# Optimization experiments

Measured on AMD Instinct MI355X. Metric: run time of the kernel, lower is better.

## Reference

```python
import jax, jax.numpy as jnp
import numpy as np

D = 1024
N_HEAD = 16
D_HEAD = D // N_HEAD
EPS = 1e-6


def setup_inputs() -> dict:
    key = jax.random.key(0)
    k1, k2, k3 = jax.random.split(key, 3)
    x = jax.random.normal(k1, (4, 1024, D), dtype=jnp.float32)
    # Linear weights stored as (in, out); y = x @ W
    Wqkv = jax.random.normal(k2, (D, 3 * D), dtype=jnp.float32) * (1.0 / np.sqrt(D))
    Wo = jax.random.normal(k3, (D, D), dtype=jnp.float32) * (1.0 / np.sqrt(D))
    scale_q = jnp.ones((D_HEAD,), dtype=jnp.float32)
    scale_k = jnp.ones((D_HEAD,), dtype=jnp.float32)
    return {"x": x, "Wqkv": Wqkv, "Wo": Wo, "scale_q": scale_q, "scale_k": scale_k}


def _rmsnorm_global(x, scale):
    # NOTE: faithful to source: mean over ALL elements (scalar RMS), not per-vector.
    rms = jnp.sqrt(jnp.mean(x * x))
    return (x / (rms + EPS)) * scale  # scale broadcasts over last dim (d_head)


def reference(x, Wqkv, Wo, scale_q, scale_k):
    b, s, d = x.shape
    qkv = x @ Wqkv  # (b, s, 3d)
    q, k, v = jnp.split(qkv, 3, axis=-1)
    q = q.reshape(b, s, N_HEAD, D_HEAD)
    k = k.reshape(b, s, N_HEAD, D_HEAD)
    v = v.reshape(b, s, N_HEAD, D_HEAD)
    q = _rmsnorm_global(q, scale_q)
    k = _rmsnorm_global(k, scale_k)
    # NOTE: no 1/sqrt(d_head) scaling, no mask (faithful to source)
    attn = jnp.einsum('bqhd,bkhd->bhqk', q, k)
    attn = jax.nn.softmax(attn, axis=-1)
    z = jnp.einsum('bhqk,bkhd->bqhd', attn, v)
    z = z.reshape(b, s, d)
    return z @ Wo
```

## Files before the change

kernel.cpp:

```cpp
#include <hip/hip_runtime.h>

typedef float f32x4 __attribute__((ext_vector_type(4)));
typedef short bf16x8 __attribute__((ext_vector_type(8)));
typedef _Float16 f16x8 __attribute__((ext_vector_type(8)));
typedef unsigned short u16;

__device__ __forceinline__ u16 f2bf(float f) {
  unsigned int u = __float_as_uint(f);
  u = u + 0x7fffu + ((u >> 16) & 1u);
  return (u16)(u >> 16);
}
__device__ __forceinline__ float bf2f(u16 h) {
  return __uint_as_float(((unsigned int)h) << 16);
}
__device__ __forceinline__ u16 f2h(float f) {
  _Float16 h = (_Float16)f;
  union { _Float16 h; u16 u; } cv;
  cv.h = h;
  return cv.u;
}

typedef unsigned int as1_uint __attribute__((address_space(1)));
typedef unsigned int as3_uint __attribute__((address_space(3)));
__device__ __forceinline__ void gl_lds16(const void* g, void* l) {
  __builtin_amdgcn_global_load_lds((as1_uint*)g, (as3_uint*)l, 16, 0, 0);
}


__global__ __launch_bounds__(256) void conv_x_kernel(const float* __restrict__ x,
                                                     u16* __restrict__ Xp) {
  const int g = blockIdx.x * 256 + threadIdx.x;
  const int o = g * 8;
  const int slab = o >> 17;
  const int rem = o & 131071;
  const int kstep = rem >> 12;
  const int rem2 = rem & 4095;
  const int r = rem2 >> 5;
  const int cp = (rem2 & 31) >> 3;
  const int c = cp ^ ((r >> 1) & 3);
  const int s = slab * 128 + r;
  const int k = kstep * 32 + c * 8;
  const float4 v0 = *(const float4*)&x[(size_t)s * 1024 + k];
  const float4 v1 = *(const float4*)&x[(size_t)s * 1024 + k + 4];
  ushort4 a, b;
  a.x = f2h(v0.x); a.y = f2h(v0.y); a.z = f2h(v0.z); a.w = f2h(v0.w);
  b.x = f2h(v1.x); b.y = f2h(v1.y); b.z = f2h(v1.z); b.w = f2h(v1.w);
  *(ushort4*)&Xp[o] = a;
  *(ushort4*)&Xp[o + 4] = b;
}

__global__ __launch_bounds__(256) void conv_w_kernel(
    const float* __restrict__ src, int ncols, u16* __restrict__ dst) {
  __shared__ float tl[64][132];
  const int t = threadIdx.x;
  const int slab = blockIdx.x, kg = blockIdx.y;
  const int n0 = slab * 128, k0 = kg * 64;
#pragma unroll
  for (int i = 0; i < 8; i++) {
    const int fidx = i * 256 + t;
    const int r = fidx >> 5, c4 = (fidx & 31) * 4;
    *(float4*)&tl[r][c4] = *(const float4*)&src[(size_t)(k0 + r) * ncols + n0 + c4];
  }
  __syncthreads();
  const size_t base = (size_t)slab * 131072 + (size_t)(kg * 2) * 4096;
#pragma unroll
  for (int i = 0; i < 4; i++) {
    const int g = i * 256 + t;
    const int img = g >> 9, ci = g & 511;
    const int r = ci >> 2, cp = ci & 3;
    const int c = cp ^ ((r >> 1) & 3);
    const int klc = img * 32 + c * 8;
    ushort4 h0, h1;
    float v[8];
#pragma unroll
    for (int e = 0; e < 8; e++) v[e] = tl[klc + e][r];
    h0.x = f2h(v[0]); h0.y = f2h(v[1]); h0.z = f2h(v[2]); h0.w = f2h(v[3]);
    h1.x = f2h(v[4]); h1.y = f2h(v[5]); h1.z = f2h(v[6]); h1.w = f2h(v[7]);
    *(ushort4*)&dst[base + g * 8] = h0;
    *(ushort4*)&dst[base + g * 8 + 4] = h1;
  }
}

__global__ __launch_bounds__(512, 2) void gemm_qkv_kernel(
    const u16* __restrict__ Xp, const u16* __restrict__ Wp,
    u16* __restrict__ qf, u16* __restrict__ kf, u16* __restrict__ vT,
    const float* __restrict__ scale_q, const float* __restrict__ scale_k,
    float* __restrict__ sums) {
  __shared__ u16 SA[2][4][4096];
  __shared__ u16 SB[2][4][4096];
  const int tid = threadIdx.x, wv = tid >> 6, lane = tid & 63;
  const int lm = lane & 15, quad = lane >> 4;
  const int wvM = wv >> 2, wvN = wv & 3;
  const int L = blockIdx.x;
  const int xcd = L & 7, idx = L >> 3;
  const int bmT = (xcd & 3) * 4 + (idx & 3);
  const int bnT = (xcd >> 2) * 6 + (idx >> 2);
  const bool is_v = (bnT >= 8);
  const int fq = (quad ^ ((lm >> 1) & 3)) * 8;
  const int aOff = lm * 32 + fq;
  const u16* Xg = Xp + (size_t)bmT * 262144;
  const u16* Wg = Wp + (size_t)bnT * 262144;
  int bSub[4];
#pragma unroll
  for (int n = 0; n < 4; n++) {
    const int wn = wvN * 64 + n * 16;
    bSub[n] = ((wn >> 7) * 4096) + (wn & 127) * 32;
  }
  const u16* Ard = is_v ? &SA[0][0][0] : &SB[0][0][0];
  const u16* Brd = is_v ? &SB[0][0][0] : &SA[0][0][0];

  const f32x4 z4 = {0.f, 0.f, 0.f, 0.f};
  f32x4 acc[8][4];
#pragma unroll
  for (int i = 0; i < 8; i++)
#pragma unroll
    for (int j = 0; j < 4; j++) acc[i][j] = z4;

#define VMCNT4() asm volatile("s_waitcnt vmcnt(4)" ::: "memory")
#define VMCNT0() asm volatile("s_waitcnt vmcnt(0)" ::: "memory")
#define LGKM0() asm volatile("s_waitcnt lgkmcnt(0)" ::: "memory")
#define CFENCE() asm volatile("" ::: "memory")
#define SP1() __builtin_amdgcn_s_setprio(1)
#define SP0() __builtin_amdgcn_s_setprio(0)

#define QSTAGE(tt, nb, k2, sl)                                               \
  do {                                                                       \
    const size_t go_ = (size_t)(sl)*131072 + (size_t)(2 * (tt) + (k2)) * 4096\
                       + wv * 512 + lane * 8;                                \
    gl_lds16(Xg + go_, &SA[nb][(k2)*2 + (sl)][wv * 512]);                    \
    gl_lds16(Wg + go_, &SB[nb][(k2)*2 + (sl)][wv * 512]);                    \
  } while (0)

#define READ_A(BUF, k2, mq)                                                  \
  _Pragma("unroll")                                                          \
  for (int i = 0; i < 4; i++)                                                \
    afr[i] = *(const f16x8*)&Ard[(BUF)*16384 + ((k2)*2 + wvM) * 4096 +       \
                                 ((mq)*4 + i) * 512 + aOff];
#define READ_B(BUF, k2)                                                      \
  _Pragma("unroll")                                                          \
  for (int n = 0; n < 4; n++)                                                \
    bfr[n] = *(const f16x8*)&Brd[(BUF)*16384 + (k2)*8192 + bSub[n] + aOff];
#define MFMA16(mq)                                                           \
  _Pragma("unroll")                                                          \
  for (int i = 0; i < 4; i++)                                                \
    _Pragma("unroll")                                                        \
    for (int n = 0; n < 4; n++)                                              \
      acc[(mq)*4 + i][n] = __builtin_amdgcn_mfma_f32_16x16x32_f16(           \
          afr[i], bfr[n], acc[(mq)*4 + i][n], 0, 0, 0);

#define PH_WAIT_MFMA(mq)                                                     \
  CFENCE();                                                                  \
  __builtin_amdgcn_s_barrier();                                              \
  CFENCE();                                                                  \
  LGKM0();                                                                   \
  __builtin_amdgcn_sched_barrier(0);                                         \
  SP1();                                                                     \
  MFMA16(mq);                                                                \
  SP0()

#define KTILE(BUF, NBUF, t, DOSTAGE, GATE1, GATE3)                           \
  do {                                                                       \
    f16x8 bfr[4];                                                            \
    {                                                  \
      f16x8 afr[4];                                                          \
      READ_A(BUF, 0, 0);                                                     \
      READ_B(BUF, 0);                                                        \
      if (DOSTAGE) QSTAGE((t) + 1, NBUF, 0, 0);                              \
      PH_WAIT_MFMA(0);                                                       \
    }                                                                        \
    {                                                 \
      f16x8 afr[4];                                                          \
      READ_A(BUF, 0, 1);                                                     \
      if (DOSTAGE) QSTAGE((t) + 1, NBUF, 0, 1);                              \
      GATE1;        \
      PH_WAIT_MFMA(1);                                                       \
    }                                                                        \
    {                                                  \
      f16x8 afr[4];                                                          \
      READ_A(BUF, 1, 0);                                                     \
      READ_B(BUF, 1);                                                        \
      if (DOSTAGE) QSTAGE((t) + 1, NBUF, 1, 0);                              \
      PH_WAIT_MFMA(0);                                                       \
    }                                                                        \
    {                                                 \
      f16x8 afr[4];                                                          \
      READ_A(BUF, 1, 1);                                                     \
      if (DOSTAGE) QSTAGE((t) + 1, NBUF, 1, 1);                              \
      GATE3;   \
      PH_WAIT_MFMA(1);                                                       \
    }                                                                        \
    \
    \
    CFENCE();                                                                \
    __builtin_amdgcn_s_barrier();                                            \
    CFENCE();                                                                \
  } while (0)

  QSTAGE(0, 0, 0, 0);
  QSTAGE(0, 0, 0, 1);
  QSTAGE(0, 0, 1, 0);
  QSTAGE(0, 0, 1, 1);
  VMCNT4();
  __builtin_amdgcn_s_barrier();
  CFENCE();
#pragma unroll 1
  for (int t = 0; t < 14; t += 2) {
    KTILE(0, 1, t, true, VMCNT4(), VMCNT4());
    KTILE(1, 0, t + 1, true, VMCNT4(), VMCNT4());
  }
  KTILE(0, 1, 14, true, VMCNT4(), VMCNT4());
  KTILE(1, 0, 15, false, VMCNT0(), (void)0);
#undef KTILE
#undef PH_WAIT_MFMA
#undef READ_A
#undef READ_B
#undef MFMA16
#undef QSTAGE

  const int bn = bnT * 256, bm = bmT * 256;
  if (!is_v) {
    const bool is_k = (bnT >= 4);
    u16* dst = is_k ? kf : qf;
    float ss = 0.f;
#pragma unroll
    for (int mi = 0; mi < 8; mi++) {
      const int col0 = bn + wvM * 128 + mi * 16 + quad * 4;
      const int hh = (col0 >> 6) & 15, d0 = col0 & 63;
      const int dhi = d0 >> 5, cc = (d0 & 31) >> 3, eo = d0 & 7;
      float sc[4] = {1.f, 1.f, 1.f, 1.f};
      if (is_k) {
        const float4 sq = *(const float4*)&scale_q[d0];
        const float4 sk = *(const float4*)&scale_k[d0];
        sc[0] = sq.x * sk.x; sc[1] = sq.y * sk.y;
        sc[2] = sq.z * sk.z; sc[3] = sq.w * sk.w;
      }
#pragma unroll
      for (int ni = 0; ni < 4; ni++) {
        const int s = bm + wvN * 64 + ni * 16 + lm;
        const int b = s >> 10, sl = s & 1023, st = sl >> 6, r = sl & 63;
        const size_t off = ((size_t)((b * 16 + hh) * 16 + st)) * 4096 +
                           dhi * 2048 + r * 32 + ((cc ^ ((r >> 1) & 3)) * 8) + eo;
        ushort4 h4;
#pragma unroll
        for (int i = 0; i < 4; i++) {
          const float a = acc[mi][ni][i];
          ss += a * a;
          const u16 hv = f2h(a * sc[i]);
          if (i == 0) h4.x = hv;
          else if (i == 1) h4.y = hv;
          else if (i == 2) h4.z = hv;
          else h4.w = hv;
        }
        *(ushort4*)&dst[off] = h4;
      }
    }
#pragma unroll
    for (int m = 32; m >= 1; m >>= 1) ss += __shfl_xor(ss, m, 64);
    if (lane == 0) atomicAdd(&sums[is_k ? 1 : 0], ss);
  } else {
#pragma unroll
    for (int ni = 0; ni < 4; ni++) {
      const int col = (bn - 2048) + wvN * 64 + ni * 16 + lm;
      const int d = col & 63, hh = col >> 6;
#pragma unroll
      for (int mi = 0; mi < 8; mi++) {
        const int s0 = bm + wvM * 128 + mi * 16 + quad * 4;
        const int b = s0 >> 10, sl = s0 & 1023, st = sl >> 6;
        const int sh = (sl & 63) >> 5, cc = (sl & 31) >> 3, eo = sl & 7;
        const size_t off = ((size_t)((b * 16 + hh) * 16 + st)) * 4096 +
                           sh * 2048 + d * 32 + ((cc ^ ((d >> 1) & 3)) * 8) + eo;
        ushort4 v4;
        v4.x = f2bf(acc[mi][ni][0]);
        v4.y = f2bf(acc[mi][ni][1]);
        v4.z = f2bf(acc[mi][ni][2]);
        v4.w = f2bf(acc[mi][ni][3]);
        *(ushort4*)&vT[off] = v4;
      }
    }
  }
#undef VMCNT4
#undef VMCNT0
#undef LGKM0
#undef CFENCE
#undef SP1
#undef SP0
}

__global__ __launch_bounds__(256) void attn_kernel(
    const u16* __restrict__ qf, const u16* __restrict__ kf,
    const u16* __restrict__ vT, const float* __restrict__ sums,
    u16* __restrict__ z) {
  __shared__ u16 pb[2][4][2][16][64];
  const int tid = threadIdx.x, wv = tid >> 6, lane = tid & 63;
  const int lm = lane & 15, quad = lane >> 4;
  const int fq = (quad ^ ((lm >> 1) & 3)) * 8;
  const int L = blockIdx.x;
  const int xcd = L & 7, idx = L >> 3;
  const int qt8 = idx & 7, p = idx >> 3;
  const int pair = xcd * 8 + p;
  const int hh = pair & 15, b = pair >> 4;
  const float inv_rq = 1.f / (sqrtf(sums[0] * (1.f / 4194304.f)) + 1e-6f);
  const float inv_rk = 1.f / (sqrtf(sums[1] * (1.f / 4194304.f)) + 1e-6f);
  const float cs = inv_rq * inv_rk;
  const size_t hb = ((size_t)(b * 16 + hh)) * 65536;
  const u16* Kg = kf + hb;
  const u16* Vg = vT + hb;

  f16x8 aF[2][2];
#pragma unroll
  for (int qs = 0; qs < 2; qs++) {
    const int soff = wv * 32 + qs * 16;
    const size_t qb = hb + (size_t)(qt8 * 2 + (soff >> 6)) * 4096 +
                      (size_t)((soff & 63) + lm) * 32 + fq;
    aF[qs][0] = *(const f16x8*)&qf[qb];
    aF[qs][1] = *(const f16x8*)&qf[qb + 2048];
  }
  const f32x4 zz = {0.f, 0.f, 0.f, 0.f};
  f32x4 zac[2][4];
#pragma unroll
  for (int qs = 0; qs < 2; qs++)
#pragma unroll
    for (int dt = 0; dt < 4; dt++) zac[qs][dt] = zz;
  float rs[2] = {0.f, 0.f};

#pragma unroll 2
  for (int it = 0; it < 16; ++it) {
    const int par = it & 1;
    const u16* Kt = Kg + (size_t)it * 4096;
    const u16* Vt = Vg + (size_t)it * 4096;
    f16x8 kf0[4], kf1[4];
    bf16x8 bv[2][4];
#pragma unroll
    for (int nt = 0; nt < 4; nt++) {
      const int ro = (nt * 16 + lm) * 32 + fq;
      kf0[nt] = *(const f16x8*)&Kt[ro];
      kf1[nt] = *(const f16x8*)&Kt[2048 + ro];
    }
#pragma unroll
    for (int ch = 0; ch < 2; ch++)
#pragma unroll
      for (int dt = 0; dt < 4; dt++)
        bv[ch][dt] = *(const bf16x8*)&Vt[ch * 2048 + (dt * 16 + lm) * 32 + fq];
#pragma unroll
    for (int qs = 0; qs < 2; qs++) {
#pragma unroll
      for (int nt = 0; nt < 4; nt++) {
        f32x4 c = zz;
        c = __builtin_amdgcn_mfma_f32_16x16x32_f16(kf0[nt], aF[qs][0], c, 0, 0, 0);
        c = __builtin_amdgcn_mfma_f32_16x16x32_f16(kf1[nt], aF[qs][1], c, 0, 0, 0);
        const int k4 = nt * 4 + quad;
        const int sw = (k4 & 8) | ((k4 ^ lm) & 7);
        ushort4 pw;
        float p0 = __expf(c[0] * cs - 60.f);
        float p1 = __expf(c[1] * cs - 60.f);
        float p2 = __expf(c[2] * cs - 60.f);
        float p3 = __expf(c[3] * cs - 60.f);
        rs[qs] += (p0 + p1) + (p2 + p3);
        pw.x = f2bf(p0); pw.y = f2bf(p1); pw.z = f2bf(p2); pw.w = f2bf(p3);
        *(ushort4*)&pb[par][wv][qs][lm][sw * 4] = pw;
      }
    }
#pragma unroll
    for (int ch = 0; ch < 2; ch++) {
#pragma unroll
      for (int qs = 0; qs < 2; qs++) {
        const int k4a = ch * 8 + quad * 2, k4b = k4a + 1;
        const ushort4 lo4 =
            *(const ushort4*)&pb[par][wv][qs][lm][((k4a & 8) | ((k4a ^ lm) & 7)) * 4];
        const ushort4 hi4 =
            *(const ushort4*)&pb[par][wv][qs][lm][((k4b & 8) | ((k4b ^ lm) & 7)) * 4];
        bf16x8 ap;
        ap[0] = (short)lo4.x; ap[1] = (short)lo4.y;
        ap[2] = (short)lo4.z; ap[3] = (short)lo4.w;
        ap[4] = (short)hi4.x; ap[5] = (short)hi4.y;
        ap[6] = (short)hi4.z; ap[7] = (short)hi4.w;
#pragma unroll
        for (int dt = 0; dt < 4; dt++)
          zac[qs][dt] = __builtin_amdgcn_mfma_f32_16x16x32_bf16(
              bv[ch][dt], ap, zac[qs][dt], 0, 0, 0);
      }
    }
  }

#pragma unroll
  for (int qs = 0; qs < 2; qs++) {
    rs[qs] += __shfl_xor(rs[qs], 16, 64);
    rs[qs] += __shfl_xor(rs[qs], 32, 64);
  }
  const int slab = b * 8 + qt8;
#pragma unroll
  for (int qs = 0; qs < 2; qs++) {
    const float inv = 1.f / rs[qs];
    const int r = wv * 32 + qs * 16 + lm;
#pragma unroll
    for (int dt = 0; dt < 4; dt++) {
      const int kstep = hh * 2 + (dt >> 1);
      const int d0 = dt * 16 + quad * 4;
      const int cc = (d0 & 31) >> 3, eo = d0 & 7;
      const size_t off = ((size_t)(slab * 32 + kstep)) * 4096 + r * 32 +
                         ((cc ^ ((r >> 1) & 3)) * 8) + eo;
      ushort4 o;
      o.x = f2h(zac[qs][dt][0] * inv);
      o.y = f2h(zac[qs][dt][1] * inv);
      o.z = f2h(zac[qs][dt][2] * inv);
      o.w = f2h(zac[qs][dt][3] * inv);
      *(ushort4*)&z[off] = o;
    }
  }
}

__global__ __launch_bounds__(256) void gemm_o_kernel(const u16* __restrict__ Wop,
                                                     const u16* __restrict__ zp,
                                                     float* __restrict__ out) {
  __shared__ u16 As0[4096], Bs0[4096], As1[4096], Bs1[4096];
  const int tid = threadIdx.x, wv = tid >> 6, lane = tid & 63;
  const int lm = lane & 15, quad = lane >> 4;
  const int wr = (wv >> 1) * 64, wc = (wv & 1) * 64;
  const int fq = (quad ^ ((lm >> 1) & 3)) * 8;
  const int L = blockIdx.x;
  const int xcd = L & 7, idx = L >> 3;
  const int rr = idx & 7, cc8 = idx >> 3;
  const int zpS = (xcd & 3) * 8 + rr;
  const int woS = (xcd >> 2) * 4 + cc8;
  const u16* Ag = Wop + (size_t)woS * 131072;
  const u16* Bg = zp + (size_t)zpS * 131072;
  const int dof0 = (wv * 2) * 512, dof1 = (wv * 2 + 1) * 512;
  const f32x4 z4 = {0.f, 0.f, 0.f, 0.f};
  f32x4 acc[4][4];
#pragma unroll
  for (int i = 0; i < 4; i++)
#pragma unroll
    for (int j = 0; j < 4; j++) acc[i][j] = z4;

#define ISSUE(t, As, Bs)                                   \
  do {                                                     \
    const size_t tb_ = (size_t)(t) * 4096;                 \
    gl_lds16(Ag + tb_ + dof0 + lane * 8, &As[dof0]);       \
    gl_lds16(Ag + tb_ + dof1 + lane * 8, &As[dof1]);       \
    gl_lds16(Bg + tb_ + dof0 + lane * 8, &Bs[dof0]);       \
    gl_lds16(Bg + tb_ + dof1 + lane * 8, &Bs[dof1]);       \
  } while (0)
#define GBODY(As, Bs)                                                     \
  do {                                                                    \
    f16x8 afr[4], bfr[4];                                                 \
_Pragma("unroll")                                                         \
    for (int mi = 0; mi < 4; mi++)                                        \
      afr[mi] = *(const f16x8*)&As[(wr + mi * 16 + lm) * 32 + fq];        \
_Pragma("unroll")                                                         \
    for (int ni = 0; ni < 4; ni++)                                        \
      bfr[ni] = *(const f16x8*)&Bs[(wc + ni * 16 + lm) * 32 + fq];        \
    DO_ISSUE;                                                             \
_Pragma("unroll")                                                         \
    for (int mi = 0; mi < 4; mi++)                                        \
_Pragma("unroll")                                                         \
      for (int ni = 0; ni < 4; ni++)                                      \
        acc[mi][ni] = __builtin_amdgcn_mfma_f32_16x16x32_f16(             \
            afr[mi], bfr[ni], acc[mi][ni], 0, 0, 0);                      \
  } while (0)

  ISSUE(0, As0, Bs0);
  for (int t = 0; t < 32; t += 2) {
    __syncthreads();
#define DO_ISSUE ISSUE(t + 1, As1, Bs1)
    GBODY(As0, Bs0);
#undef DO_ISSUE
    __syncthreads();
#define DO_ISSUE if (t + 2 < 32) ISSUE(t + 2, As0, Bs0)
    GBODY(As1, Bs1);
#undef DO_ISSUE
  }
#undef ISSUE
#undef GBODY

#pragma unroll
  for (int mi = 0; mi < 4; mi++) {
    const int col0 = woS * 128 + wr + mi * 16 + quad * 4;
#pragma unroll
    for (int ni = 0; ni < 4; ni++) {
      const int s = zpS * 128 + wc + ni * 16 + lm;
      const float4 o = {acc[mi][ni][0], acc[mi][ni][1], acc[mi][ni][2],
                        acc[mi][ni][3]};
      *(float4*)&out[(size_t)s * 1024 + col0] = o;
    }
  }
}

extern "C" void kernel_launch(void* const* d_in, const int* in_sizes, int n_in,
                              void* d_out, int out_size, void* d_ws,
                              size_t ws_size, hipStream_t stream) {
  (void)in_sizes; (void)n_in; (void)out_size; (void)ws_size;
  const float* x = (const float*)d_in[0];
  const float* Wqkv = (const float*)d_in[1];
  const float* Wo = (const float*)d_in[2];
  const float* scale_q = (const float*)d_in[3];
  const float* scale_k = (const float*)d_in[4];
  float* out = (float*)d_out;

  char* ws = (char*)d_ws;
  u16* qf = (u16*)(ws + 0);
  u16* kf = (u16*)(ws + 8388608);
  u16* Xp = (u16*)(ws + 16777216);
  u16* vT = (u16*)(ws + 25165824);
  u16* Wp = (u16*)(ws + 33554432);
  u16* zp = Xp;
  u16* Wop = Wp;
  float* sums = (float*)(ws + 39845888);

  conv_x_kernel<<<2048, 256, 0, stream>>>(x, Xp);
  conv_w_kernel<<<dim3(24, 16), 256, 0, stream>>>(Wqkv, 3072, Wp);
  hipMemsetAsync(sums, 0, 2 * sizeof(float), stream);
  gemm_qkv_kernel<<<192, 512, 0, stream>>>(Xp, Wp, qf, kf, vT,
                                           scale_q, scale_k, sums);
  conv_w_kernel<<<dim3(8, 16), 256, 0, stream>>>(Wo, 1024, Wop);
  attn_kernel<<<512, 256, 0, stream>>>(qf, kf, vT, sums, zp);
  gemm_o_kernel<<<256, 256, 0, stream>>>(Wop, zp, out);
}
```

Measured before the change: 184.2 us.

## Halve attention query tile per block and hoist Wo conversion before QKV GEMM

Each attention block now handles a 64-row query tile (16 rows per wave) instead of 128, and the grid doubles to 1024 blocks with a launch-bounds occupancy hint of 4. The aim is more parallelism and fewer registers per thread so more waves fit per CU. The cost is that each K/V tile is loaded twice as often across blocks. Separately, the Wo conversion gets its own workspace buffer and moves ahead of the QKV GEMM, so it no longer sits between the GEMM and the attention kernel.

```diff
diff --git a/kernel.cpp b/kernel.cpp
--- a/kernel.cpp
+++ b/kernel.cpp
@@ -286,17 +286,17 @@
 #undef SP0
 }
 
-__global__ __launch_bounds__(256) void attn_kernel(
+__global__ __launch_bounds__(256, 4) void attn_kernel(
     const u16* __restrict__ qf, const u16* __restrict__ kf,
     const u16* __restrict__ vT, const float* __restrict__ sums,
     u16* __restrict__ z) {
-  __shared__ u16 pb[2][4][2][16][64];
+  __shared__ u16 pb[2][4][16][64];
   const int tid = threadIdx.x, wv = tid >> 6, lane = tid & 63;
   const int lm = lane & 15, quad = lane >> 4;
   const int fq = (quad ^ ((lm >> 1) & 3)) * 8;
   const int L = blockIdx.x;
   const int xcd = L & 7, idx = L >> 3;
-  const int qt8 = idx & 7, p = idx >> 3;
+  const int qt = idx & 15, p = idx >> 4;
   const int pair = xcd * 8 + p;
   const int hh = pair & 15, b = pair >> 4;
   const float inv_rq = 1.f / (sqrtf(sums[0] * (1.f / 4194304.f)) + 1e-6f);
@@ -306,22 +306,17 @@
   const u16* Kg = kf + hb;
   const u16* Vg = vT + hb;
 
-  f16x8 aF[2][2];
-#pragma unroll
-  for (int qs = 0; qs < 2; qs++) {
-    const int soff = wv * 32 + qs * 16;
-    const size_t qb = hb + (size_t)(qt8 * 2 + (soff >> 6)) * 4096 +
-                      (size_t)((soff & 63) + lm) * 32 + fq;
-    aF[qs][0] = *(const f16x8*)&qf[qb];
-    aF[qs][1] = *(const f16x8*)&qf[qb + 2048];
+  f16x8 aF[2];
+  {
+    const size_t qb = hb + (size_t)qt * 4096 + (size_t)(wv * 16 + lm) * 32 + fq;
+    aF[0] = *(const f16x8*)&qf[qb];
+    aF[1] = *(const f16x8*)&qf[qb + 2048];
   }
   const f32x4 zz = {0.f, 0.f, 0.f, 0.f};
-  f32x4 zac[2][4];
-#pragma unroll
-  for (int qs = 0; qs < 2; qs++)
-#pragma unroll
-    for (int dt = 0; dt < 4; dt++) zac[qs][dt] = zz;
-  float rs[2] = {0.f, 0.f};
+  f32x4 zac[4];
+#pragma unroll
+  for (int dt = 0; dt < 4; dt++) zac[dt] = zz;
+  float rs = 0.f;
 
 #pragma unroll 2
   for (int it = 0; it < 16; ++it) {
@@ -342,70 +337,58 @@
       for (int dt = 0; dt < 4; dt++)
         bv[ch][dt] = *(const bf16x8*)&Vt[ch * 2048 + (dt * 16 + lm) * 32 + fq];
 #pragma unroll
-    for (int qs = 0; qs < 2; qs++) {
-#pragma unroll
-      for (int nt = 0; nt < 4; nt++) {
-        f32x4 c = zz;
-        c = __builtin_amdgcn_mfma_f32_16x16x32_f16(kf0[nt], aF[qs][0], c, 0, 0, 0);
-        c = __builtin_amdgcn_mfma_f32_16x16x32_f16(kf1[nt], aF[qs][1], c, 0, 0, 0);
-        const int k4 = nt * 4 + quad;
-        const int sw = (k4 & 8) | ((k4 ^ lm) & 7);
-        ushort4 pw;
-        float p0 = __expf(c[0] * cs - 60.f);
-        float p1 = __expf(c[1] * cs - 60.f);
-        float p2 = __expf(c[2] * cs - 60.f);
-        float p3 = __expf(c[3] * cs - 60.f);
-        rs[qs] += (p0 + p1) + (p2 + p3);
-        pw.x = f2bf(p0); pw.y = f2bf(p1); pw.z = f2bf(p2); pw.w = f2bf(p3);
-        *(ushort4*)&pb[par][wv][qs][lm][sw * 4] = pw;
-      }
+    for (int nt = 0; nt < 4; nt++) {
+      f32x4 c = zz;
+      c = __builtin_amdgcn_mfma_f32_16x16x32_f16(kf0[nt], aF[0], c, 0, 0, 0);
+      c = __builtin_amdgcn_mfma_f32_16x16x32_f16(kf1[nt], aF[1], c, 0, 0, 0);
+      const int k4 = nt * 4 + quad;
+      const int sw = (k4 & 8) | ((k4 ^ lm) & 7);
+      ushort4 pw;
+      float p0 = __expf(c[0] * cs - 60.f);
+      float p1 = __expf(c[1] * cs - 60.f);
+      float p2 = __expf(c[2] * cs - 60.f);
+      float p3 = __expf(c[3] * cs - 60.f);
+      rs += (p0 + p1) + (p2 + p3);
+      pw.x = f2bf(p0); pw.y = f2bf(p1); pw.z = f2bf(p2); pw.w = f2bf(p3);
+      *(ushort4*)&pb[par][wv][lm][sw * 4] = pw;
     }
 #pragma unroll
     for (int ch = 0; ch < 2; ch++) {
-#pragma unroll
-      for (int qs = 0; qs < 2; qs++) {
-        const int k4a = ch * 8 + quad * 2, k4b = k4a + 1;
-        const ushort4 lo4 =
-            *(const ushort4*)&pb[par][wv][qs][lm][((k4a & 8) | ((k4a ^ lm) & 7)) * 4];
-        const ushort4 hi4 =
-            *(const ushort4*)&pb[par][wv][qs][lm][((k4b & 8) | ((k4b ^ lm) & 7)) * 4];
-        bf16x8 ap;
-        ap[0] = (short)lo4.x; ap[1] = (short)lo4.y;
-        ap[2] = (short)lo4.z; ap[3] = (short)lo4.w;
-        ap[4] = (short)hi4.x; ap[5] = (short)hi4.y;
-        ap[6] = (short)hi4.z; ap[7] = (short)hi4.w;
-#pragma unroll
-        for (int dt = 0; dt < 4; dt++)
-          zac[qs][dt] = __builtin_amdgcn_mfma_f32_16x16x32_bf16(
-              bv[ch][dt], ap, zac[qs][dt], 0, 0, 0);
-      }
+      const int k4a = ch * 8 + quad * 2, k4b = k4a + 1;
+      const ushort4 lo4 =
+          *(const ushort4*)&pb[par][wv][lm][((k4a & 8) | ((k4a ^ lm) & 7)) * 4];
+      const ushort4 hi4 =
+          *(const ushort4*)&pb[par][wv][lm][((k4b & 8) | ((k4b ^ lm) & 7)) * 4];
+      bf16x8 ap;
+      ap[0] = (short)lo4.x; ap[1] = (short)lo4.y;
+      ap[2] = (short)lo4.z; ap[3] = (short)lo4.w;
+      ap[4] = (short)hi4.x; ap[5] = (short)hi4.y;
+      ap[6] = (short)hi4.z; ap[7] = (short)hi4.w;
+#pragma unroll
+      for (int dt = 0; dt < 4; dt++)
+        zac[dt] = __builtin_amdgcn_mfma_f32_16x16x32_bf16(
+            bv[ch][dt], ap, zac[dt], 0, 0, 0);
     }
   }
 
-#pragma unroll
-  for (int qs = 0; qs < 2; qs++) {
-    rs[qs] += __shfl_xor(rs[qs], 16, 64);
-    rs[qs] += __shfl_xor(rs[qs], 32, 64);
-  }
-  const int slab = b * 8 + qt8;
-#pragma unroll
-  for (int qs = 0; qs < 2; qs++) {
-    const float inv = 1.f / rs[qs];
-    const int r = wv * 32 + qs * 16 + lm;
-#pragma unroll
-    for (int dt = 0; dt < 4; dt++) {
-      const int kstep = hh * 2 + (dt >> 1);
-      const int d0 = dt * 16 + quad * 4;
-      const int cc = (d0 & 31) >> 3, eo = d0 & 7;
-      const size_t off = ((size_t)(slab * 32 + kstep)) * 4096 + r * 32 +
-                         ((cc ^ ((r >> 1) & 3)) * 8) + eo;
-      ushort4 o;
-      o.x = f2h(zac[qs][dt][0] * inv);
-      o.y = f2h(zac[qs][dt][1] * inv);
-      o.z = f2h(zac[qs][dt][2] * inv);
-      o.w = f2h(zac[qs][dt][3] * inv);
-      *(ushort4*)&z[off] = o;
-    }
+  rs += __shfl_xor(rs, 16, 64);
+  rs += __shfl_xor(rs, 32, 64);
+  const float inv = 1.f / rs;
+  const int slab = b * 8 + (qt >> 1);
+  const int r = (qt & 1) * 64 + wv * 16 + lm;
+#pragma unroll
+  for (int dt = 0; dt < 4; dt++) {
+    const int kstep = hh * 2 + (dt >> 1);
+    const int d0 = dt * 16 + quad * 4;
+    const int cc = (d0 & 31) >> 3, eo = d0 & 7;
+    const size_t off = ((size_t)(slab * 32 + kstep)) * 4096 + r * 32 +
+                       ((cc ^ ((r >> 1) & 3)) * 8) + eo;
+    ushort4 o;
+    o.x = f2h(zac[dt][0] * inv);
+    o.y = f2h(zac[dt][1] * inv);
+    o.z = f2h(zac[dt][2] * inv);
+    o.w = f2h(zac[dt][3] * inv);
+    *(ushort4*)&z[off] = o;
   }
 }
 
@@ -502,16 +485,16 @@
   u16* Xp = (u16*)(ws + 16777216);
   u16* vT = (u16*)(ws + 25165824);
   u16* Wp = (u16*)(ws + 33554432);
+  float* sums = (float*)(ws + 39845888);
+  u16* Wop = (u16*)(ws + 41943040);
   u16* zp = Xp;
-  u16* Wop = Wp;
-  float* sums = (float*)(ws + 39845888);
 
   conv_x_kernel<<<2048, 256, 0, stream>>>(x, Xp);
   conv_w_kernel<<<dim3(24, 16), 256, 0, stream>>>(Wqkv, 3072, Wp);
+  conv_w_kernel<<<dim3(8, 16), 256, 0, stream>>>(Wo, 1024, Wop);
   hipMemsetAsync(sums, 0, 2 * sizeof(float), stream);
   gemm_qkv_kernel<<<192, 512, 0, stream>>>(Xp, Wp, qf, kf, vT,
                                            scale_q, scale_k, sums);
-  conv_w_kernel<<<dim3(8, 16), 256, 0, stream>>>(Wo, 1024, Wop);
-  attn_kernel<<<512, 256, 0, stream>>>(qf, kf, vT, sums, zp);
+  attn_kernel<<<1024, 256, 0, stream>>>(qf, kf, vT, sums, zp);
   gemm_o_kernel<<<256, 256, 0, stream>>>(Wop, zp, out);
 }
```

Result: no change. 187.8 us (+2.0%).
